# Kernel optimization log

Hardware: AMD Instinct MI355X
Metric: run time of the kernel (lower is better)

## Reference

```python
import jax, jax.numpy as jnp
import numpy as np
from jax import lax

B, S, D, H = 131072, 4, 128, 1


def setup_inputs() -> dict:
    key = jax.random.key(0)
    k1, k2, k3, k4 = jax.random.split(key, 4)
    x = jax.random.normal(k1, (B, S, D), dtype=jnp.float32)
    # reset_parameters uses torch.rand -> uniform [0,1)
    weight = jax.random.uniform(k2, (D, H), dtype=jnp.float32)
    weight_h = jax.random.uniform(k3, (1, H), dtype=jnp.float32)
    bias = jax.random.uniform(k4, (1,), dtype=jnp.float32)
    return {"x": x, "weight": weight, "weight_h": weight_h, "bias": bias}


def reference(x, weight, weight_h, bias):
    # batch_first: x -> [S, B, D]; only x[0, t, :] is used, t in range(B).
    # Recurrence: y_t = bias + x[0, t] @ weight + y_{t-1} * weight_h, y_{-1} = 0.
    u = x[:, 0, :] @ weight + bias  # [B, H] precomputed input drive
    wh = weight_h[0]                # [H]

    def step(y_prev, u_t):
        y = u_t + y_prev * wh
        return y, y

    y_last, ys = lax.scan(step, jnp.zeros((weight.shape[1],), x.dtype), u)
    h_n = ys                        # [B, H] with H == 1 -> matches h_n [batch, 1]
    y_h = y_last[None, :]           # [1, H]
    return h_n, y_h, y_h
```

## Files before the change

### kernel.cpp

```cpp
#include <hip/hip_runtime.h>


#define B_ROWS 131072
#define CHUNK  256
#define NCHUNK 512
#define MAGIC  0x7C3A9E51u

template <int CTRL>
__device__ __forceinline__ float dpp_add(float s) {
    int v = __builtin_amdgcn_update_dpp(0, __builtin_bit_cast(int, s), CTRL, 0xF, 0xF, true);
    return s + __builtin_bit_cast(float, v);
}

__global__ __launch_bounds__(256) void k_dot(const float* __restrict__ x,
                                             const float* __restrict__ w,
                                             const float* __restrict__ bias,
                                             float* __restrict__ u) {
    const int gtid = blockIdx.x * 256 + threadIdx.x;
    const int wave = gtid >> 6;
    const int lane = threadIdx.x & 63;
    const int half = lane >> 5;
    const int hl   = lane & 31;
    const float4 wv = *reinterpret_cast<const float4*>(w + hl * 4);
    const float  bs = bias[0];
    const int rbase = wave * 2 + half;

    float4 xv[8];
#pragma unroll
    for (int r = 0; r < 8; ++r) {
        const int row = rbase + r * 16384;
        xv[r] = *reinterpret_cast<const float4*>(x + (size_t)row * 512 + hl * 4);
    }
#pragma unroll
    for (int r = 0; r < 8; ++r) {
        float s = fmaf(xv[r].x, wv.x, fmaf(xv[r].y, wv.y,
                  fmaf(xv[r].z, wv.z, xv[r].w * wv.w)));
        s = dpp_add<0xB1>(s);
        s = dpp_add<0x4E>(s);
        s = dpp_add<0x141>(s);
        s = dpp_add<0x140>(s);
        s += __shfl_xor(s, 16, 64);
        if (hl == 0) u[rbase + r * 16384] = s + bs;
    }
}

__global__ __launch_bounds__(256) void k_scan_apply(const float* __restrict__ u,
                                                    const float* __restrict__ wh_p,
                                                    unsigned long long* __restrict__ pk,
                                                    float* __restrict__ out) {
    __shared__ float wl[4];
    __shared__ float Sw[8];
    __shared__ float ex_s;
    const int tid  = threadIdx.x;
    const int wv   = tid >> 6;
    const int lane = tid & 63;
    const int k    = blockIdx.x;
    const int base = k * CHUNK;

    const float a = wh_p[0];
    float c = u[base + tid];
    float fstep = a;
#pragma unroll
    for (int s = 1; s < 64; s <<= 1) {
        float prev = __shfl_up(c, (unsigned)s, 64);
        if (lane >= s) c = fmaf(prev, fstep, c);
        fstep *= fstep;
    }
    const float f64 = fstep;
    float apw = a, bse = a;
#pragma unroll
    for (int b = 0; b < 6; ++b) { if (lane & (1 << b)) apw *= bse; bse *= bse; }

    if (lane == 63) wl[wv] = c;
    __syncthreads();
    if (wv > 0) {
        float seed = wl[0];
#pragma unroll
        for (int j = 1; j < 4; ++j) if (j < wv) seed = fmaf(seed, f64, wl[j]);
        c = fmaf(seed, apw, c);
    }

    if (tid == CHUNK - 1) {
        unsigned long long q =
            ((unsigned long long)__float_as_uint(c) << 32) | (unsigned long long)MAGIC;
        __hip_atomic_store(&pk[k], q, __ATOMIC_RELAXED, __HIP_MEMORY_SCOPE_AGENT);
    }

    const float Af = [&]{ float t2 = f64 * f64; return t2 * t2; }();
    const int nw = (k + 63) >> 6;
    for (int wi = wv; wi < nw; wi += 4) {
        const int j0 = wi << 6;
        const int t  = min(64, k - j0);
        float cj = 0.0f;
        if (lane < t) {
            unsigned long long q = __hip_atomic_load(&pk[j0 + lane], __ATOMIC_RELAXED,
                                                     __HIP_MEMORY_SCOPE_AGENT);
            while ((unsigned int)q != MAGIC) {
                __builtin_amdgcn_s_sleep(1);
                q = __hip_atomic_load(&pk[j0 + lane], __ATOMIC_RELAXED,
                                      __HIP_MEMORY_SCOPE_AGENT);
            }
            cj = __uint_as_float((unsigned int)(q >> 32));
        }
        float P = cj, ff = Af;
#pragma unroll
        for (int s = 1; s < 64; s <<= 1) {
            float prev = __shfl_up(P, (unsigned)s, 64);
            if (lane >= s) P = fmaf(prev, ff, P);
            ff *= ff;
        }
        if (lane == t - 1) Sw[wi] = P;
    }
    __syncthreads();

    if (tid == 0) {
        float ex = 0.0f;
        if (nw > 0) {
            float A64 = Af;
#pragma unroll
            for (int i = 0; i < 6; ++i) A64 *= A64;
            for (int wi = 0; wi < nw - 1; ++wi) ex = fmaf(ex, A64, Sw[wi]);
            const int tl = k - ((nw - 1) << 6);
            float At = 1.0f, bb = Af;
#pragma unroll
            for (int b = 0; b < 7; ++b) { if (tl & (1 << b)) At *= bb; bb *= bb; }
            ex = fmaf(ex, At, Sw[nw - 1]);
        }
        ex_s = ex;
    }
    __syncthreads();

    const float ex = ex_s;
    float pw = apw;
#pragma unroll
    for (int j = 0; j < 4; ++j) if (j < wv) pw *= f64;
    const float y = fmaf(pw, ex, c);
    out[base + tid] = y;
    if (k == NCHUNK - 1 && tid == CHUNK - 1) {
        out[B_ROWS]     = y;
        out[B_ROWS + 1] = y;
    }
}

extern "C" void kernel_launch(void* const* d_in, const int* in_sizes, int n_in,
                              void* d_out, int out_size, void* d_ws, size_t ws_size,
                              hipStream_t stream) {
    const float* x    = (const float*)d_in[0];
    const float* w    = (const float*)d_in[1];
    const float* wh   = (const float*)d_in[2];
    const float* bias = (const float*)d_in[3];
    float* out = (float*)d_out;

    float* u               = (float*)d_ws;
    unsigned long long* pk = (unsigned long long*)(u + B_ROWS);

    k_dot<<<2048, 256, 0, stream>>>(x, w, bias, u);
    k_scan_apply<<<NCHUNK, 256, 0, stream>>>(u, wh, pk, out);
}
```

Before: 21.47 us.

## Fuse dot and scan kernels into one launch with per-element flag handoff

Merges the dot-product pass and the chunked scan into a single grid. The first 2048 blocks compute the drive values and publish each one as a value plus magic-tag 64-bit word. The remaining 512 blocks spin on those words before starting their scan, which removes the kernel-boundary drain and the second launch. Row mapping also changes so each wave handles 16 contiguous rows, letting a scan chunk depend on a small number of dot blocks. The risks are doubled workspace traffic from the 8-byte words, spin-wait overhead, and reliance on dot blocks being scheduled before or alongside the scan blocks to avoid deadlock.

```diff
diff --git a/kernel.cpp b/kernel.cpp
--- a/kernel.cpp
+++ b/kernel.cpp
@@ -4,12 +4,154 @@
 #define B_ROWS 131072
 #define CHUNK  256
 #define NCHUNK 512
+#define NDOT   2048
 #define MAGIC  0x7C3A9E51u
 
 template <int CTRL>
 __device__ __forceinline__ float dpp_add(float s) {
     int v = __builtin_amdgcn_update_dpp(0, __builtin_bit_cast(int, s), CTRL, 0xF, 0xF, true);
     return s + __builtin_bit_cast(float, v);
+}
+
+__device__ __forceinline__ unsigned long long pack_val(float v) {
+    return ((unsigned long long)__float_as_uint(v) << 32) | (unsigned long long)MAGIC;
+}
+
+__global__ __launch_bounds__(256, 8) void k_all(const float* __restrict__ x,
+                                                const float* __restrict__ w,
+                                                const float* __restrict__ wh_p,
+                                                const float* __restrict__ bias,
+                                                float* __restrict__ out,
+                                                unsigned long long* __restrict__ uq,
+                                                unsigned long long* __restrict__ pk) {
+    const int tid  = threadIdx.x;
+    const int lane = tid & 63;
+
+    if (blockIdx.x < NDOT) {
+        const int wave = ((int)blockIdx.x * 256 + tid) >> 6;
+        const int half = lane >> 5;
+        const int hl   = lane & 31;
+        const float4 wvec = *reinterpret_cast<const float4*>(w + hl * 4);
+        const float  bs   = bias[0];
+        const int row0 = wave * 16;
+        float4 xv[8];
+#pragma unroll
+        for (int r = 0; r < 8; ++r) {
+            const int row = row0 + r * 2 + half;
+            xv[r] = *reinterpret_cast<const float4*>(x + (size_t)row * 512 + hl * 4);
+        }
+#pragma unroll
+        for (int r = 0; r < 8; ++r) {
+            float s = fmaf(xv[r].x, wvec.x, fmaf(xv[r].y, wvec.y,
+                      fmaf(xv[r].z, wvec.z, xv[r].w * wvec.w)));
+            s = dpp_add<0xB1>(s);
+            s = dpp_add<0x4E>(s);
+            s = dpp_add<0x141>(s);
+            s = dpp_add<0x140>(s);
+            s += __shfl_xor(s, 16, 64);
+            if (hl == 0)
+                __hip_atomic_store(&uq[row0 + r * 2 + half], pack_val(s + bs),
+                                   __ATOMIC_RELAXED, __HIP_MEMORY_SCOPE_AGENT);
+        }
+        return;
+    }
+
+    __shared__ float wl[4];
+    __shared__ float Sw[8];
+    __shared__ float ex_s;
+    const int wv   = tid >> 6;
+    const int k    = (int)blockIdx.x - NDOT;
+    const int base = k * CHUNK;
+
+    unsigned long long q = __hip_atomic_load(&uq[base + tid], __ATOMIC_RELAXED,
+                                             __HIP_MEMORY_SCOPE_AGENT);
+    while ((unsigned int)q != MAGIC) {
+        __builtin_amdgcn_s_sleep(2);
+        q = __hip_atomic_load(&uq[base + tid], __ATOMIC_RELAXED,
+                              __HIP_MEMORY_SCOPE_AGENT);
+    }
+    float c = __uint_as_float((unsigned int)(q >> 32));
+
+    const float a = wh_p[0];
+    float fstep = a;
+#pragma unroll
+    for (int s = 1; s < 64; s <<= 1) {
+        float prev = __shfl_up(c, (unsigned)s, 64);
+        if (lane >= s) c = fmaf(prev, fstep, c);
+        fstep *= fstep;
+    }
+    const float f64 = fstep;
+    float apw = a, bse = a;
+#pragma unroll
+    for (int b = 0; b < 6; ++b) { if (lane & (1 << b)) apw *= bse; bse *= bse; }
+
+    if (lane == 63) wl[wv] = c;
+    __syncthreads();
+    if (wv > 0) {
+        float seed = wl[0];
+#pragma unroll
+        for (int j = 1; j < 4; ++j) if (j < wv) seed = fmaf(seed, f64, wl[j]);
+        c = fmaf(seed, apw, c);
+    }
+
+    if (tid == CHUNK - 1)
+        __hip_atomic_store(&pk[k], pack_val(c), __ATOMIC_RELAXED,
+                           __HIP_MEMORY_SCOPE_AGENT);
+
+    const float Af = [&]{ float t2 = f64 * f64; return t2 * t2; }();
+    const int nw = (k + 63) >> 6;
+    for (int wi = wv; wi < nw; wi += 4) {
+        const int j0 = wi << 6;
+        const int t  = min(64, k - j0);
+        float cj = 0.0f;
+        if (lane < t) {
+            unsigned long long qq = __hip_atomic_load(&pk[j0 + lane], __ATOMIC_RELAXED,
+                                                      __HIP_MEMORY_SCOPE_AGENT);
+            while ((unsigned int)qq != MAGIC) {
+                __builtin_amdgcn_s_sleep(1);
+                qq = __hip_atomic_load(&pk[j0 + lane], __ATOMIC_RELAXED,
+                                       __HIP_MEMORY_SCOPE_AGENT);
+            }
+            cj = __uint_as_float((unsigned int)(qq >> 32));
+        }
+        float P = cj, ff = Af;
+#pragma unroll
+        for (int s = 1; s < 64; s <<= 1) {
+            float prev = __shfl_up(P, (unsigned)s, 64);
+            if (lane >= s) P = fmaf(prev, ff, P);
+            ff *= ff;
+        }
+        if (lane == t - 1) Sw[wi] = P;
+    }
+    __syncthreads();
+
+    if (tid == 0) {
+        float ex = 0.0f;
+        if (nw > 0) {
+            float A64 = Af;
+#pragma unroll
+            for (int i = 0; i < 6; ++i) A64 *= A64;
+            for (int wi = 0; wi < nw - 1; ++wi) ex = fmaf(ex, A64, Sw[wi]);
+            const int tl = k - ((nw - 1) << 6);
+            float At = 1.0f, bb = Af;
+#pragma unroll
+            for (int b = 0; b < 7; ++b) { if (tl & (1 << b)) At *= bb; bb *= bb; }
+            ex = fmaf(ex, At, Sw[nw - 1]);
+        }
+        ex_s = ex;
+    }
+    __syncthreads();
+
+    const float ex = ex_s;
+    float pw = apw;
+#pragma unroll
+    for (int j = 0; j < 4; ++j) if (j < wv) pw *= f64;
+    const float y = fmaf(pw, ex, c);
+    out[base + tid] = y;
+    if (k == NCHUNK - 1 && tid == CHUNK - 1) {
+        out[B_ROWS]     = y;
+        out[B_ROWS + 1] = y;
+    }
 }
 
 __global__ __launch_bounds__(256) void k_dot(const float* __restrict__ x,
@@ -23,24 +165,19 @@
     const int hl   = lane & 31;
     const float4 wv = *reinterpret_cast<const float4*>(w + hl * 4);
     const float  bs = bias[0];
-    const int rbase = wave * 2 + half;
-
+    const int row0 = wave * 16;
     float4 xv[8];
 #pragma unroll
-    for (int r = 0; r < 8; ++r) {
-        const int row = rbase + r * 16384;
-        xv[r] = *reinterpret_cast<const float4*>(x + (size_t)row * 512 + hl * 4);
-    }
+    for (int r = 0; r < 8; ++r)
+        xv[r] = *reinterpret_cast<const float4*>(x + (size_t)(row0 + r * 2 + half) * 512 + hl * 4);
 #pragma unroll
     for (int r = 0; r < 8; ++r) {
         float s = fmaf(xv[r].x, wv.x, fmaf(xv[r].y, wv.y,
                   fmaf(xv[r].z, wv.z, xv[r].w * wv.w)));
-        s = dpp_add<0xB1>(s);
-        s = dpp_add<0x4E>(s);
-        s = dpp_add<0x141>(s);
-        s = dpp_add<0x140>(s);
+        s = dpp_add<0xB1>(s); s = dpp_add<0x4E>(s);
+        s = dpp_add<0x141>(s); s = dpp_add<0x140>(s);
         s += __shfl_xor(s, 16, 64);
-        if (hl == 0) u[rbase + r * 16384] = s + bs;
+        if (hl == 0) u[row0 + r * 2 + half] = s + bs;
     }
 }
 
@@ -79,12 +216,9 @@
         for (int j = 1; j < 4; ++j) if (j < wv) seed = fmaf(seed, f64, wl[j]);
         c = fmaf(seed, apw, c);
     }
-
-    if (tid == CHUNK - 1) {
-        unsigned long long q =
-            ((unsigned long long)__float_as_uint(c) << 32) | (unsigned long long)MAGIC;
-        __hip_atomic_store(&pk[k], q, __ATOMIC_RELAXED, __HIP_MEMORY_SCOPE_AGENT);
-    }
+    if (tid == CHUNK - 1)
+        __hip_atomic_store(&pk[k], pack_val(c), __ATOMIC_RELAXED,
+                           __HIP_MEMORY_SCOPE_AGENT);
 
     const float Af = [&]{ float t2 = f64 * f64; return t2 * t2; }();
     const int nw = (k + 63) >> 6;
@@ -93,14 +227,14 @@
         const int t  = min(64, k - j0);
         float cj = 0.0f;
         if (lane < t) {
-            unsigned long long q = __hip_atomic_load(&pk[j0 + lane], __ATOMIC_RELAXED,
-                                                     __HIP_MEMORY_SCOPE_AGENT);
-            while ((unsigned int)q != MAGIC) {
+            unsigned long long qq = __hip_atomic_load(&pk[j0 + lane], __ATOMIC_RELAXED,
+                                                      __HIP_MEMORY_SCOPE_AGENT);
+            while ((unsigned int)qq != MAGIC) {
                 __builtin_amdgcn_s_sleep(1);
-                q = __hip_atomic_load(&pk[j0 + lane], __ATOMIC_RELAXED,
-                                      __HIP_MEMORY_SCOPE_AGENT);
+                qq = __hip_atomic_load(&pk[j0 + lane], __ATOMIC_RELAXED,
+                                       __HIP_MEMORY_SCOPE_AGENT);
             }
-            cj = __uint_as_float((unsigned int)(q >> 32));
+            cj = __uint_as_float((unsigned int)(qq >> 32));
         }
         float P = cj, ff = Af;
 #pragma unroll
@@ -151,9 +285,15 @@
     const float* bias = (const float*)d_in[3];
     float* out = (float*)d_out;
 
-    float* u               = (float*)d_ws;
-    unsigned long long* pk = (unsigned long long*)(u + B_ROWS);
-
-    k_dot<<<2048, 256, 0, stream>>>(x, w, bias, u);
-    k_scan_apply<<<NCHUNK, 256, 0, stream>>>(u, wh, pk, out);
-}
+    const size_t need = (size_t)B_ROWS * 8 + (size_t)NCHUNK * 8;
+    if (ws_size >= need) {
+        unsigned long long* uq = (unsigned long long*)d_ws;
+        unsigned long long* pk = uq + B_ROWS;
+        k_all<<<NDOT + NCHUNK, 256, 0, stream>>>(x, w, wh, bias, out, uq, pk);
+    } else {
+        float* u               = (float*)d_ws;
+        unsigned long long* pk = (unsigned long long*)(u + B_ROWS);
+        k_dot<<<NDOT, 256, 0, stream>>>(x, w, bias, u);
+        k_scan_apply<<<NCHUNK, 256, 0, stream>>>(u, wh, pk, out);
+    }
+}
```

Measured after the change: 20.23 us. 5.7% less time.
